# Kernel tuning notes

Hardware: AMD Instinct MI355X
Metric: run time of the kernel (lower is better)

## Reference

```python
import jax, jax.numpy as jnp
import numpy as np

N = 50000
E = 800000
NEG_SLOPE = 0.2


def gat_conv(x, W, att_src, att_dst, bias, src, dst, concat):
    """PyG GATConv (shared lin for src/dst, self-loops already included in src/dst).
    x: [N, Fin], W: [Fin, H*C], att_*: [H, C], bias: [H*C] if concat else [C].
    """
    H, C = att_src.shape
    h = (x @ W).reshape(N, H, C)                      # [N,H,C]
    a_src = jnp.sum(h * att_src[None], axis=-1)       # [N,H]
    a_dst = jnp.sum(h * att_dst[None], axis=-1)       # [N,H]
    alpha = a_src[src] + a_dst[dst]                   # [E,H]
    alpha = jax.nn.leaky_relu(alpha, NEG_SLOPE)
    # segment softmax over incoming edges of each destination node
    amax = jax.ops.segment_max(alpha, dst, num_segments=N)
    alpha = jnp.exp(alpha - amax[dst])
    denom = jax.ops.segment_sum(alpha, dst, num_segments=N)
    alpha = alpha / (denom[dst] + 1e-16)
    msg = h[src] * alpha[:, :, None]                  # [E,H,C]
    out = jax.ops.segment_sum(msg, dst, num_segments=N)  # [N,H,C]
    if concat:
        return out.reshape(N, H * C) + bias
    return out.mean(axis=1) + bias


def setup_inputs() -> dict:
    key = jax.random.key(0)
    ks = jax.random.split(key, 10)
    x = jax.random.normal(ks[0], (N, 64), dtype=jnp.float32)
    edge_index = jax.random.randint(ks[1], (2, E), 0, N, dtype=jnp.int32)
    s = 0.1
    # layer 1: in=64 -> heads=2, out=32, concat=True (width 64)
    W1 = jax.random.normal(ks[2], (64, 64), dtype=jnp.float32) * s
    att_src1 = jax.random.normal(ks[3], (2, 32), dtype=jnp.float32) * s
    att_dst1 = jax.random.normal(ks[4], (2, 32), dtype=jnp.float32) * s
    b1 = jnp.zeros((64,), dtype=jnp.float32)
    # recon: in=64 -> heads=2, out=64, concat=False
    W2 = jax.random.normal(ks[5], (64, 128), dtype=jnp.float32) * s
    att_src2 = jax.random.normal(ks[6], (2, 64), dtype=jnp.float32) * s
    att_dst2 = jax.random.normal(ks[7], (2, 64), dtype=jnp.float32) * s
    b2 = jnp.zeros((64,), dtype=jnp.float32)
    return {"x": x, "edge_index": edge_index,
            "W1": W1, "att_src1": att_src1, "att_dst1": att_dst1, "b1": b1,
            "W2": W2, "att_src2": att_src2, "att_dst2": att_dst2, "b2": b2}


def reference(x, edge_index, W1, att_src1, att_dst1, b1, W2, att_src2, att_dst2, b2):
    # add self loops (PyG GATConv default)
    loop = jnp.arange(N, dtype=edge_index.dtype)
    src = jnp.concatenate([edge_index[0], loop])
    dst = jnp.concatenate([edge_index[1], loop])
    h = gat_conv(x, W1, att_src1, att_dst1, b1, src, dst, concat=True)
    out = gat_conv(h, W2, att_src2, att_dst2, b2, src, dst, concat=False)
    return out
```

## Files before the change

### kernel.cpp

```cpp
#include <hip/hip_runtime.h>
#include <hip/hip_fp16.h>

#define NEG_SLOPE 0.2f
#define BCAP 6144

__device__ __forceinline__ float lrelu(float a) { return a > 0.f ? a : NEG_SLOPE * a; }

struct half4 { __half2 a, b; };
__device__ __forceinline__ half4 pack_half4(float4 v) {
    half4 r; r.a = __floats2half2_rn(v.x, v.y); r.b = __floats2half2_rn(v.z, v.w); return r;
}
__device__ __forceinline__ void unpack8(uint4 u, float* f) {
    const __half2* hp = (const __half2*)&u;
#pragma unroll
    for (int i = 0; i < 4; i++) {
        float2 t = __half22float2(hp[i]);
        f[2 * i] = t.x; f[2 * i + 1] = t.y;
    }
}
__device__ __forceinline__ void unpack4(uint2 u, float* f) {
    const __half2* hp = (const __half2*)&u;
#pragma unroll
    for (int i = 0; i < 2; i++) {
        float2 t = __half22float2(hp[i]);
        f[2 * i] = t.x; f[2 * i + 1] = t.y;
    }
}
__device__ __forceinline__ uint2 pack_half4f(const float* f) {
    uint2 u;
    __half2* hp = (__half2*)&u;
    hp[0] = __floats2half2_rn(f[0], f[1]);
    hp[1] = __floats2half2_rn(f[2], f[3]);
    return u;
}


__global__ __launch_bounds__(256) void init_va_kernel(int* __restrict__ bcur, int NBK,
                                                      const float* __restrict__ W2,
                                                      const float* __restrict__ att_s,
                                                      const float* __restrict__ att_d,
                                                      float* __restrict__ va_s,
                                                      float* __restrict__ va_d) {
    int t = threadIdx.x;
    if (t < NBK) bcur[t] = t * BCAP;
    int which = t >> 7;
    int h = (t >> 6) & 1, k = t & 63;
    const float* att = which ? att_d : att_s;
    float acc = 0.f;
    for (int c = 0; c < 64; c++)
        acc += W2[k * 128 + h * 64 + c] * att[h * 64 + c];
    (which ? va_d : va_s)[h * 64 + k] = acc;
}

__global__ __launch_bounds__(256) void bucketA_kernel(const int* __restrict__ ei, int E,
                                                      int Etot, int* __restrict__ bcur,
                                                      uint2* __restrict__ btmp) {
    __shared__ int lh[256];
    __shared__ int lbase[256];
    int t = threadIdx.x;
    int b0 = blockIdx.x * 4096;
    lh[t] = 0;
    __syncthreads();
    int s[16], d[16], bk[16];
#pragma unroll
    for (int i = 0; i < 16; i++) {
        int e = b0 + i * 256 + t;
        if (e < Etot) {
            int ss, dd;
            if (e < E) { ss = ei[e]; dd = ei[E + e]; }
            else       { ss = e - E; dd = ss; }
            s[i] = ss; d[i] = dd; bk[i] = dd >> 8;
            atomicAdd(&lh[bk[i]], 1);
        } else bk[i] = -1;
    }
    __syncthreads();
    if (lh[t] > 0) lbase[t] = atomicAdd(&bcur[t], lh[t]);
    __syncthreads();
    lh[t] = 0;
    __syncthreads();
#pragma unroll
    for (int i = 0; i < 16; i++) {
        if (bk[i] >= 0) {
            int pos = lbase[bk[i]] + atomicAdd(&lh[bk[i]], 1);
            btmp[pos] = make_uint2((unsigned)s[i], (unsigned)d[i]);
        }
    }
}

__global__ __launch_bounds__(256) void bucketB_kernel(const uint2* __restrict__ btmp,
                                                      const int* __restrict__ bcur,
                                                      int N, uint2* __restrict__ rowinfo,
                                                      int* __restrict__ csr) {
    __shared__ int lh[256];
    __shared__ int lbase[256];
    __shared__ int wsum[4];
    int bkt = blockIdx.x;
    int n0 = bkt << 8;
    int n1 = n0 + 256; if (n1 > N) n1 = N;
    int nn = n1 - n0;
    int t = threadIdx.x;
    lh[t] = 0;
    __syncthreads();
    int ebeg = bkt * BCAP;
    int eend = bcur[bkt];
    for (int e = ebeg + t; e < eend; e += 256)
        atomicAdd(&lh[(int)btmp[e].y - n0], 1);
    __syncthreads();
    int v = lh[t];
    int s = v;
    int lane = t & 63, w = t >> 6;
#pragma unroll
    for (int off = 1; off < 64; off <<= 1) {
        int x = __shfl_up(s, off, 64);
        if (lane >= off) s += x;
    }
    if (lane == 63) wsum[w] = s;
    __syncthreads();
    int woff = 0;
    if (w > 0) woff += wsum[0];
    if (w > 1) woff += wsum[1];
    if (w > 2) woff += wsum[2];
    int excl = woff + s - v;
    lbase[t] = ebeg + excl;
    if (t < nn) rowinfo[n0 + t] = make_uint2((unsigned)(ebeg + excl), (unsigned)v);
    lh[t] = 0;
    __syncthreads();
    for (int e = ebeg + t; e < eend; e += 256) {
        uint2 sd = btmp[e];
        int dl = (int)sd.y - n0;
        int slot = atomicAdd(&lh[dl], 1);
        csr[lbase[dl] + slot] = (int)sd.x;
    }
}


template <int M>
__global__ __launch_bounds__(256) void gemm64_kernel(const float* __restrict__ X,
                                                     const float* __restrict__ W,
                                                     __half* __restrict__ Yh,
                                                     const float* __restrict__ att_s,
                                                     const float* __restrict__ att_d,
                                                     float* __restrict__ a_src,
                                                     float* __restrict__ a_dst, int N) {
    constexpr int CG = M / 4;
    constexpr int RB = (256 / CG) * 2;
    constexpr int HL = CG / 2;
    __shared__ float4 ws[64 * CG];
    __shared__ float  xs[RB][68];
    int t = threadIdx.x;
    for (int i = t; i < 64 * CG; i += 256) ws[i] = ((const float4*)W)[i];
    int r0 = blockIdx.x * RB;
    for (int i = t; i < RB * 16; i += 256) {
        int r = i >> 4, k4 = i & 15;
        int row = r0 + r;
        float4 v = (row < N) ? ((const float4*)X)[(size_t)row * 16 + k4]
                             : make_float4(0.f, 0.f, 0.f, 0.f);
        ((float4*)&xs[r][0])[k4] = v;
    }
    __syncthreads();
    int c = t % CG;
    int rl = (t / CG) * 2;
    float4 a0 = make_float4(0.f, 0.f, 0.f, 0.f);
    float4 a1 = make_float4(0.f, 0.f, 0.f, 0.f);
#pragma unroll 8
    for (int k = 0; k < 64; k++) {
        float4 w = ws[k * CG + c];
        float x0 = xs[rl][k];
        float x1 = xs[rl + 1][k];
        a0.x = fmaf(x0, w.x, a0.x); a0.y = fmaf(x0, w.y, a0.y);
        a0.z = fmaf(x0, w.z, a0.z); a0.w = fmaf(x0, w.w, a0.w);
        a1.x = fmaf(x1, w.x, a1.x); a1.y = fmaf(x1, w.y, a1.y);
        a1.z = fmaf(x1, w.z, a1.z); a1.w = fmaf(x1, w.w, a1.w);
    }
    int row0 = r0 + rl;
    if (row0 < N)     ((half4*)Yh)[(size_t)row0 * CG + c] = pack_half4(a0);
    if (row0 + 1 < N) ((half4*)Yh)[(size_t)(row0 + 1) * CG + c] = pack_half4(a1);

    float4 s4 = ((const float4*)att_s)[c];
    float4 d4 = ((const float4*)att_d)[c];
    float vs0 = a0.x * s4.x + a0.y * s4.y + a0.z * s4.z + a0.w * s4.w;
    float vd0 = a0.x * d4.x + a0.y * d4.y + a0.z * d4.z + a0.w * d4.w;
    float vs1 = a1.x * s4.x + a1.y * s4.y + a1.z * s4.z + a1.w * s4.w;
    float vd1 = a1.x * d4.x + a1.y * d4.y + a1.z * d4.z + a1.w * d4.w;
#pragma unroll
    for (int off = 1; off < HL; off <<= 1) {
        vs0 += __shfl_xor(vs0, off, 64);
        vd0 += __shfl_xor(vd0, off, 64);
        vs1 += __shfl_xor(vs1, off, 64);
        vd1 += __shfl_xor(vd1, off, 64);
    }
    if ((c & (HL - 1)) == 0) {
        int hh = c / HL;
        if (row0 < N)     { a_src[row0 * 2 + hh] = vs0; a_dst[row0 * 2 + hh] = vd0; }
        if (row0 + 1 < N) { a_src[(row0 + 1) * 2 + hh] = vs1; a_dst[(row0 + 1) * 2 + hh] = vd1; }
    }
}


__device__ __forceinline__ void reg_softmax64(const float* __restrict__ asrc, float2 ad,
                                              const int* __restrict__ csr, int beg, int deg,
                                              int lane, int& sidx, float& w0n, float& w1n) {
    float a0 = -1e30f, a1 = -1e30f;
    sidx = 0;
    if (lane < deg) {
        sidx = csr[beg + lane];
        float2 as = ((const float2*)asrc)[sidx];
        a0 = lrelu(as.x + ad.x);
        a1 = lrelu(as.y + ad.y);
    }
    float m0 = a0, m1 = a1;
#pragma unroll
    for (int off = 32; off; off >>= 1) {
        m0 = fmaxf(m0, __shfl_xor(m0, off, 64));
        m1 = fmaxf(m1, __shfl_xor(m1, off, 64));
    }
    float w0 = (lane < deg) ? __expf(a0 - m0) : 0.f;
    float w1 = (lane < deg) ? __expf(a1 - m1) : 0.f;
    float d0 = w0, d1 = w1;
#pragma unroll
    for (int off = 32; off; off >>= 1) {
        d0 += __shfl_xor(d0, off, 64);
        d1 += __shfl_xor(d1, off, 64);
    }
    w0n = w0 / (d0 + 1e-16f);
    w1n = w1 / (d1 + 1e-16f);
}

__device__ __forceinline__ void reg_softmax32(const float* __restrict__ asrc, float2 ad,
                                              const int* __restrict__ csr, int beg, int deg,
                                              int hl, int& sidx, float& w0n, float& w1n) {
    float a0 = -1e30f, a1 = -1e30f;
    sidx = 0;
    if (hl < deg) {
        sidx = csr[beg + hl];
        float2 as = ((const float2*)asrc)[sidx];
        a0 = lrelu(as.x + ad.x);
        a1 = lrelu(as.y + ad.y);
    }
    float m0 = a0, m1 = a1;
#pragma unroll
    for (int off = 16; off; off >>= 1) {
        m0 = fmaxf(m0, __shfl_xor(m0, off, 64));
        m1 = fmaxf(m1, __shfl_xor(m1, off, 64));
    }
    float w0 = (hl < deg) ? __expf(a0 - m0) : 0.f;
    float w1 = (hl < deg) ? __expf(a1 - m1) : 0.f;
    float d0 = w0, d1 = w1;
#pragma unroll
    for (int off = 16; off; off >>= 1) {
        d0 += __shfl_xor(d0, off, 64);
        d1 += __shfl_xor(d1, off, 64);
    }
    w0n = w0 / (d0 + 1e-16f);
    w1n = w1 / (d1 + 1e-16f);
}


__device__ void concat_full64(const __half* __restrict__ hg, const float* __restrict__ asrc,
                              const float* __restrict__ adst, const uint2* __restrict__ rowinfo,
                              const int* __restrict__ csr, const float* __restrict__ bias,
                              __half* __restrict__ out1h, const float* __restrict__ vaS,
                              const float* __restrict__ vaD, float* __restrict__ asrc2,
                              float* __restrict__ adst2, int node, int lane) {
    uint2 ri = rowinfo[node];
    int beg = (int)ri.x, deg = (int)ri.y;
    int end = beg + deg;
    float2 ad = ((const float2*)adst)[node];
    int g = lane >> 4, q = lane & 15;
    float acc[4];
#pragma unroll
    for (int j = 0; j < 4; j++) acc[j] = 0.f;
    if (deg <= 64) {
        int sidx; float w0n, w1n;
        reg_softmax64(asrc, ad, csr, beg, deg, lane, sidx, w0n, w1n);
        for (int j0 = 0; j0 < deg; j0 += 4) {
            int j = j0 + g;
            int s = __shfl(sidx, j, 64);
            float wa = __shfl(w0n, j, 64);
            float wb = __shfl(w1n, j, 64);
            bool valid = j < deg;
            float w = valid ? ((q < 8) ? wa : wb) : 0.f;
            s = valid ? s : 0;
            uint2 u = ((const uint2*)(hg + (size_t)s * 64))[q];
            float f[4];
            unpack4(u, f);
#pragma unroll
            for (int k = 0; k < 4; k++) acc[k] = fmaf(f[k], w, acc[k]);
        }
    } else {
        float m0 = -1e30f, m1 = -1e30f;
        for (int i = lane; i < deg; i += 64) {
            int s = csr[beg + i];
            float2 as = ((const float2*)asrc)[s];
            m0 = fmaxf(m0, lrelu(as.x + ad.x));
            m1 = fmaxf(m1, lrelu(as.y + ad.y));
        }
#pragma unroll
        for (int off = 32; off; off >>= 1) {
            m0 = fmaxf(m0, __shfl_xor(m0, off, 64));
            m1 = fmaxf(m1, __shfl_xor(m1, off, 64));
        }
        float d0 = 0.f, d1 = 0.f;
        for (int i = lane; i < deg; i += 64) {
            int s = csr[beg + i];
            float2 as = ((const float2*)asrc)[s];
            d0 += __expf(lrelu(as.x + ad.x) - m0);
            d1 += __expf(lrelu(as.y + ad.y) - m1);
        }
#pragma unroll
        for (int off = 32; off; off >>= 1) {
            d0 += __shfl_xor(d0, off, 64);
            d1 += __shfl_xor(d1, off, 64);
        }
        float inv0 = 1.f / (d0 + 1e-16f), inv1 = 1.f / (d1 + 1e-16f);
        for (int e = beg + g; e < end; e += 4) {
            int s = csr[e];
            float2 as = ((const float2*)asrc)[s];
            float w = (q < 8) ? __expf(lrelu(as.x + ad.x) - m0) * inv0
                              : __expf(lrelu(as.y + ad.y) - m1) * inv1;
            uint2 u = ((const uint2*)(hg + (size_t)s * 64))[q];
            float f[4];
            unpack4(u, f);
#pragma unroll
            for (int k = 0; k < 4; k++) acc[k] = fmaf(f[k], w, acc[k]);
        }
    }
#pragma unroll
    for (int j = 0; j < 4; j++) {
        acc[j] += __shfl_xor(acc[j], 16, 64);
        acc[j] += __shfl_xor(acc[j], 32, 64);
    }
    float4 b = ((const float4*)bias)[q];
    acc[0] += b.x; acc[1] += b.y; acc[2] += b.z; acc[3] += b.w;
    if (lane < 16)
        ((uint2*)(out1h + (size_t)node * 64))[q] = pack_half4f(acc);
    float4 sA = ((const float4*)vaS)[q];
    float4 sB = ((const float4*)vaS)[16 + q];
    float4 dA = ((const float4*)vaD)[q];
    float4 dB = ((const float4*)vaD)[16 + q];
    float rs0 = acc[0] * sA.x + acc[1] * sA.y + acc[2] * sA.z + acc[3] * sA.w;
    float rs1 = acc[0] * sB.x + acc[1] * sB.y + acc[2] * sB.z + acc[3] * sB.w;
    float rd0 = acc[0] * dA.x + acc[1] * dA.y + acc[2] * dA.z + acc[3] * dA.w;
    float rd1 = acc[0] * dB.x + acc[1] * dB.y + acc[2] * dB.z + acc[3] * dB.w;
#pragma unroll
    for (int off = 1; off < 16; off <<= 1) {
        rs0 += __shfl_xor(rs0, off, 64);
        rs1 += __shfl_xor(rs1, off, 64);
        rd0 += __shfl_xor(rd0, off, 64);
        rd1 += __shfl_xor(rd1, off, 64);
    }
    if (lane == 0) {
        ((float2*)asrc2)[node] = make_float2(rs0, rs1);
        ((float2*)adst2)[node] = make_float2(rd0, rd1);
    }
}

__device__ void agg2_full64(const __half* __restrict__ xg, const float* __restrict__ asrc,
                            const float* __restrict__ adst, const uint2* __restrict__ rowinfo,
                            const int* __restrict__ csr, __half* __restrict__ aggcat,
                            int node, int lane) {
    uint2 ri = rowinfo[node];
    int beg = (int)ri.x, deg = (int)ri.y;
    int end = beg + deg;
    float2 ad = ((const float2*)adst)[node];
    int g = lane >> 4, q = lane & 15;
    float acc0[4], acc1[4];
#pragma unroll
    for (int j = 0; j < 4; j++) { acc0[j] = 0.f; acc1[j] = 0.f; }
    if (deg <= 64) {
        int sidx; float w0n, w1n;
        reg_softmax64(asrc, ad, csr, beg, deg, lane, sidx, w0n, w1n);
        for (int j0 = 0; j0 < deg; j0 += 4) {
            int j = j0 + g;
            int s = __shfl(sidx, j, 64);
            float wa = __shfl(w0n, j, 64);
            float wb = __shfl(w1n, j, 64);
            bool valid = j < deg;
            float w0 = valid ? wa : 0.f;
            float w1 = valid ? wb : 0.f;
            s = valid ? s : 0;
            uint2 u = ((const uint2*)(xg + (size_t)s * 64))[q];
            float f[4];
            unpack4(u, f);
#pragma unroll
            for (int k = 0; k < 4; k++) {
                acc0[k] = fmaf(f[k], w0, acc0[k]);
                acc1[k] = fmaf(f[k], w1, acc1[k]);
            }
        }
    } else {
        float m0 = -1e30f, m1 = -1e30f;
        for (int i = lane; i < deg; i += 64) {
            int s = csr[beg + i];
            float2 as = ((const float2*)asrc)[s];
            m0 = fmaxf(m0, lrelu(as.x + ad.x));
            m1 = fmaxf(m1, lrelu(as.y + ad.y));
        }
#pragma unroll
        for (int off = 32; off; off >>= 1) {
            m0 = fmaxf(m0, __shfl_xor(m0, off, 64));
            m1 = fmaxf(m1, __shfl_xor(m1, off, 64));
        }
        float d0 = 0.f, d1 = 0.f;
        for (int i = lane; i < deg; i += 64) {
            int s = csr[beg + i];
            float2 as = ((const float2*)asrc)[s];
            d0 += __expf(lrelu(as.x + ad.x) - m0);
            d1 += __expf(lrelu(as.y + ad.y) - m1);
        }
#pragma unroll
        for (int off = 32; off; off >>= 1) {
            d0 += __shfl_xor(d0, off, 64);
            d1 += __shfl_xor(d1, off, 64);
        }
        float inv0 = 1.f / (d0 + 1e-16f), inv1 = 1.f / (d1 + 1e-16f);
        for (int e = beg + g; e < end; e += 4) {
            int s = csr[e];
            float2 as = ((const float2*)asrc)[s];
            float w0 = __expf(lrelu(as.x + ad.x) - m0) * inv0;
            float w1 = __expf(lrelu(as.y + ad.y) - m1) * inv1;
            uint2 u = ((const uint2*)(xg + (size_t)s * 64))[q];
            float f[4];
            unpack4(u, f);
#pragma unroll
            for (int k = 0; k < 4; k++) {
                acc0[k] = fmaf(f[k], w0, acc0[k]);
                acc1[k] = fmaf(f[k], w1, acc1[k]);
            }
        }
    }
#pragma unroll
    for (int j = 0; j < 4; j++) {
        acc0[j] += __shfl_xor(acc0[j], 16, 64);
        acc0[j] += __shfl_xor(acc0[j], 32, 64);
        acc1[j] += __shfl_xor(acc1[j], 16, 64);
        acc1[j] += __shfl_xor(acc1[j], 32, 64);
    }
    if (lane < 16) {
        ((uint2*)(aggcat + (size_t)node * 128))[q] = pack_half4f(acc0);
        ((uint2*)(aggcat + (size_t)node * 128 + 64))[q] = pack_half4f(acc1);
    }
}


__global__ __launch_bounds__(256) void agg_sm_concat_kernel(const __half* __restrict__ hg,
                                                            const float* __restrict__ asrc,
                                                            const float* __restrict__ adst,
                                                            const uint2* __restrict__ rowinfo,
                                                            const int* __restrict__ csr,
                                                            const float* __restrict__ bias,
                                                            __half* __restrict__ out1h,
                                                            const float* __restrict__ vaS,
                                                            const float* __restrict__ vaD,
                                                            float* __restrict__ asrc2,
                                                            float* __restrict__ adst2, int N) {
    int nodeA = blockIdx.x * 8 + (threadIdx.x >> 6) * 2;
    if (nodeA >= N) return;
    int lane = threadIdx.x & 63;
    int half = lane >> 5, hl = lane & 31;
    int node = nodeA + half;
    bool nodeok = node < N;
    int nodec = nodeok ? node : nodeA;
    uint2 ri = rowinfo[nodec];
    int beg = (int)ri.x, deg = (int)ri.y;
    int degmax = max(deg, __shfl_xor(deg, 32, 64));

    if (degmax <= 32) {
        float2 ad = ((const float2*)adst)[nodec];
        int sidx; float w0n, w1n;
        reg_softmax32(asrc, ad, csr, beg, deg, hl, sidx, w0n, w1n);
        int g = hl >> 4, q = hl & 15;
        float acc[4];
#pragma unroll
        for (int j = 0; j < 4; j++) acc[j] = 0.f;
        for (int j0 = 0; j0 < degmax; j0 += 4) {
            int jA = j0 + g, jB = j0 + 2 + g;
            int slA = half * 32 + (jA < 31 ? jA : 31);
            int slB = half * 32 + (jB < 31 ? jB : 31);
            int sA = __shfl(sidx, slA, 64);
            float waA = __shfl(w0n, slA, 64);
            float wbA = __shfl(w1n, slA, 64);
            int sB = __shfl(sidx, slB, 64);
            float waB = __shfl(w0n, slB, 64);
            float wbB = __shfl(w1n, slB, 64);
            bool vA = jA < deg, vB = jB < deg;
            float wA = vA ? ((q < 8) ? waA : wbA) : 0.f;
            float wB = vB ? ((q < 8) ? waB : wbB) : 0.f;
            sA = vA ? sA : 0;
            sB = vB ? sB : 0;
            uint2 uA = ((const uint2*)(hg + (size_t)sA * 64))[q];
            uint2 uB = ((const uint2*)(hg + (size_t)sB * 64))[q];
            float fA[4], fB[4];
            unpack4(uA, fA);
            unpack4(uB, fB);
#pragma unroll
            for (int k = 0; k < 4; k++) acc[k] = fmaf(fA[k], wA, acc[k]);
#pragma unroll
            for (int k = 0; k < 4; k++) acc[k] = fmaf(fB[k], wB, acc[k]);
        }
#pragma unroll
        for (int j = 0; j < 4; j++) acc[j] += __shfl_xor(acc[j], 16, 64);
        float4 b = ((const float4*)bias)[q];
        acc[0] += b.x; acc[1] += b.y; acc[2] += b.z; acc[3] += b.w;
        if (nodeok && hl < 16)
            ((uint2*)(out1h + (size_t)node * 64))[q] = pack_half4f(acc);
        float4 sA4 = ((const float4*)vaS)[q];
        float4 sB4 = ((const float4*)vaS)[16 + q];
        float4 dA4 = ((const float4*)vaD)[q];
        float4 dB4 = ((const float4*)vaD)[16 + q];
        float rs0 = acc[0] * sA4.x + acc[1] * sA4.y + acc[2] * sA4.z + acc[3] * sA4.w;
        float rs1 = acc[0] * sB4.x + acc[1] * sB4.y + acc[2] * sB4.z + acc[3] * sB4.w;
        float rd0 = acc[0] * dA4.x + acc[1] * dA4.y + acc[2] * dA4.z + acc[3] * dA4.w;
        float rd1 = acc[0] * dB4.x + acc[1] * dB4.y + acc[2] * dB4.z + acc[3] * dB4.w;
#pragma unroll
        for (int off = 1; off < 16; off <<= 1) {
            rs0 += __shfl_xor(rs0, off, 64);
            rs1 += __shfl_xor(rs1, off, 64);
            rd0 += __shfl_xor(rd0, off, 64);
            rd1 += __shfl_xor(rd1, off, 64);
        }
        if (nodeok && hl == 0) {
            ((float2*)asrc2)[node] = make_float2(rs0, rs1);
            ((float2*)adst2)[node] = make_float2(rd0, rd1);
        }
    } else {
        concat_full64(hg, asrc, adst, rowinfo, csr, bias, out1h, vaS, vaD,
                      asrc2, adst2, nodeA, lane);
        if (nodeA + 1 < N)
            concat_full64(hg, asrc, adst, rowinfo, csr, bias, out1h, vaS, vaD,
                          asrc2, adst2, nodeA + 1, lane);
    }
}


__global__ __launch_bounds__(256) void agg_sm2_kernel(const __half* __restrict__ xg,
                                                      const float* __restrict__ asrc,
                                                      const float* __restrict__ adst,
                                                      const uint2* __restrict__ rowinfo,
                                                      const int* __restrict__ csr,
                                                      __half* __restrict__ aggcat, int N) {
    int nodeA = blockIdx.x * 8 + (threadIdx.x >> 6) * 2;
    if (nodeA >= N) return;
    int lane = threadIdx.x & 63;
    int half = lane >> 5, hl = lane & 31;
    int node = nodeA + half;
    bool nodeok = node < N;
    int nodec = nodeok ? node : nodeA;
    uint2 ri = rowinfo[nodec];
    int beg = (int)ri.x, deg = (int)ri.y;
    int degmax = max(deg, __shfl_xor(deg, 32, 64));

    if (degmax <= 32) {
        float2 ad = ((const float2*)adst)[nodec];
        int sidx; float w0n, w1n;
        reg_softmax32(asrc, ad, csr, beg, deg, hl, sidx, w0n, w1n);
        int g = hl >> 4, q = hl & 15;
        float acc0[4], acc1[4];
#pragma unroll
        for (int j = 0; j < 4; j++) { acc0[j] = 0.f; acc1[j] = 0.f; }
        for (int j0 = 0; j0 < degmax; j0 += 4) {
            int jA = j0 + g, jB = j0 + 2 + g;
            int slA = half * 32 + (jA < 31 ? jA : 31);
            int slB = half * 32 + (jB < 31 ? jB : 31);
            int sA = __shfl(sidx, slA, 64);
            float waA = __shfl(w0n, slA, 64);
            float wbA = __shfl(w1n, slA, 64);
            int sB = __shfl(sidx, slB, 64);
            float waB = __shfl(w0n, slB, 64);
            float wbB = __shfl(w1n, slB, 64);
            bool vA = jA < deg, vB = jB < deg;
            float w0A = vA ? waA : 0.f, w1A = vA ? wbA : 0.f;
            float w0B = vB ? waB : 0.f, w1B = vB ? wbB : 0.f;
            sA = vA ? sA : 0;
            sB = vB ? sB : 0;
            uint2 uA = ((const uint2*)(xg + (size_t)sA * 64))[q];
            uint2 uB = ((const uint2*)(xg + (size_t)sB * 64))[q];
            float fA[4], fB[4];
            unpack4(uA, fA);
            unpack4(uB, fB);
#pragma unroll
            for (int k = 0; k < 4; k++) {
                acc0[k] = fmaf(fA[k], w0A, acc0[k]);
                acc1[k] = fmaf(fA[k], w1A, acc1[k]);
            }
#pragma unroll
            for (int k = 0; k < 4; k++) {
                acc0[k] = fmaf(fB[k], w0B, acc0[k]);
                acc1[k] = fmaf(fB[k], w1B, acc1[k]);
            }
        }
#pragma unroll
        for (int j = 0; j < 4; j++) {
            acc0[j] += __shfl_xor(acc0[j], 16, 64);
            acc1[j] += __shfl_xor(acc1[j], 16, 64);
        }
        if (nodeok && hl < 16) {
            ((uint2*)(aggcat + (size_t)node * 128))[q] = pack_half4f(acc0);
            ((uint2*)(aggcat + (size_t)node * 128 + 64))[q] = pack_half4f(acc1);
        }
    } else {
        agg2_full64(xg, asrc, adst, rowinfo, csr, aggcat, nodeA, lane);
        if (nodeA + 1 < N)
            agg2_full64(xg, asrc, adst, rowinfo, csr, aggcat, nodeA + 1, lane);
    }
}


__global__ __launch_bounds__(256) void gemmK128_kernel(const __half* __restrict__ Xh,
                                                       const float* __restrict__ W2,
                                                       const float* __restrict__ bias,
                                                       float* __restrict__ Y, int N) {
    __shared__ float4 ws[128 * 16];
    __shared__ float  xs[32][132];
    int t = threadIdx.x;
    for (int i = t; i < 128 * 16; i += 256) {
        int k2 = i >> 4, c4 = i & 15;
        int k = k2 & 63, h = k2 >> 6;
        float4 w = ((const float4*)W2)[k * 32 + h * 16 + c4];
        w.x *= 0.5f; w.y *= 0.5f; w.z *= 0.5f; w.w *= 0.5f;
        ws[i] = w;
    }
    int r0 = blockIdx.x * 32;
    for (int i = t; i < 512; i += 256) {
        int r = i >> 4, j = i & 15;
        int row = r0 + r;
        uint4 u = make_uint4(0u, 0u, 0u, 0u);
        if (row < N) u = ((const uint4*)(Xh + (size_t)row * 128))[j];
        float f[8];
        unpack8(u, f);
#pragma unroll
        for (int jj = 0; jj < 8; jj++) xs[r][j * 8 + jj] = f[jj];
    }
    __syncthreads();
    int c = t & 15;
    int rl = (t >> 4) * 2;
    float4 a0 = make_float4(0.f, 0.f, 0.f, 0.f);
    float4 a1 = make_float4(0.f, 0.f, 0.f, 0.f);
#pragma unroll 8
    for (int k = 0; k < 128; k++) {
        float4 w = ws[k * 16 + c];
        float x0 = xs[rl][k];
        float x1 = xs[rl + 1][k];
        a0.x = fmaf(x0, w.x, a0.x); a0.y = fmaf(x0, w.y, a0.y);
        a0.z = fmaf(x0, w.z, a0.z); a0.w = fmaf(x0, w.w, a0.w);
        a1.x = fmaf(x1, w.x, a1.x); a1.y = fmaf(x1, w.y, a1.y);
        a1.z = fmaf(x1, w.z, a1.z); a1.w = fmaf(x1, w.w, a1.w);
    }
    float4 b = ((const float4*)bias)[c];
    a0.x += b.x; a0.y += b.y; a0.z += b.z; a0.w += b.w;
    a1.x += b.x; a1.y += b.y; a1.z += b.z; a1.w += b.w;
    int row0 = r0 + rl;
    if (row0 < N)     ((float4*)Y)[(size_t)row0 * 16 + c] = a0;
    if (row0 + 1 < N) ((float4*)Y)[(size_t)(row0 + 1) * 16 + c] = a1;
}


extern "C" void kernel_launch(void* const* d_in, const int* in_sizes, int n_in,
                              void* d_out, int out_size, void* d_ws, size_t ws_size,
                              hipStream_t stream) {
    const float* x        = (const float*)d_in[0];
    const int*   ei       = (const int*)d_in[1];
    const float* W1       = (const float*)d_in[2];
    const float* att_src1 = (const float*)d_in[3];
    const float* att_dst1 = (const float*)d_in[4];
    const float* b1       = (const float*)d_in[5];
    const float* W2       = (const float*)d_in[6];
    const float* att_src2 = (const float*)d_in[7];
    const float* att_dst2 = (const float*)d_in[8];
    const float* b2       = (const float*)d_in[9];
    float* out = (float*)d_out;

    const int N = in_sizes[0] / 64;
    const int E = in_sizes[1] / 2;
    const int Etot = E + N;
    const int NBK = (N + 255) >> 8;

    char* base = (char*)d_ws;
    size_t off = 0;
    auto alloc = [&](size_t bytes) -> char* {
        char* p = base + off;
        off = (off + bytes + 255) & ~(size_t)255;
        return p;
    };
    int*    bcur    = (int*)alloc((size_t)NBK * 4);
    uint2*  rowinfo = (uint2*)alloc((size_t)N * 8);
    int*    csr     = (int*)alloc((size_t)NBK * BCAP * 4);
    uint2*  btmp    = (uint2*)alloc((size_t)NBK * BCAP * 8);
    __half* h1g     = (__half*)alloc((size_t)N * 64 * 2);
    float*  asrc1   = (float*)alloc((size_t)N * 2 * 4);
    float*  adst1   = (float*)alloc((size_t)N * 2 * 4);
    __half* out1h   = (__half*)alloc((size_t)N * 64 * 2);
    __half* aggcat  = (__half*)alloc((size_t)N * 128 * 2);
    float*  asrc2   = (float*)alloc((size_t)N * 2 * 4);
    float*  adst2   = (float*)alloc((size_t)N * 2 * 4);
    float*  vaS     = (float*)alloc(128 * 4);
    float*  vaD     = (float*)alloc(128 * 4);
    (void)ws_size; (void)n_in; (void)out_size;

    const int nba = (Etot + 4095) / 4096;
    const int nb8 = (N + 7) / 8;

    init_va_kernel<<<1, 256, 0, stream>>>(bcur, NBK, W2, att_src2, att_dst2, vaS, vaD);
    bucketA_kernel<<<nba, 256, 0, stream>>>(ei, E, Etot, bcur, btmp);
    bucketB_kernel<<<NBK, 256, 0, stream>>>(btmp, bcur, N, rowinfo, csr);

    gemm64_kernel<64><<<(N + 31) / 32, 256, 0, stream>>>(x, W1, h1g, att_src1, att_dst1,
                                                         asrc1, adst1, N);
    agg_sm_concat_kernel<<<nb8, 256, 0, stream>>>(h1g, asrc1, adst1, rowinfo, csr, b1,
                                                  out1h, vaS, vaD, asrc2, adst2, N);

    agg_sm2_kernel<<<nb8, 256, 0, stream>>>(out1h, asrc2, adst2, rowinfo, csr, aggcat, N);
    gemmK128_kernel<<<(N + 31) / 32, 256, 0, stream>>>(aggcat, W2, b2, out, N);
}
```

Measured before the change: 117.8 us.

## Pack bucket edges into 32 bits, half-pack softmax weights, widen gather unroll

Bucketed edges are stored as one 32-bit word (16-bit source plus 8-bit local destination) instead of a uint2, halving the temp traffic in the CSR build. Softmax weights for both heads are packed into one fp16 pair so one shuffle replaces two. The aggregation loops now issue four neighbour row gathers per iteration instead of two, to raise memory-level parallelism. This assumes node indices fit in 16 bits and lowers weight precision to fp16.

Measured after the change: 117.5 us. About the same (-0.3%).

```diff
diff --git a/kernel.cpp b/kernel.cpp
--- a/kernel.cpp
+++ b/kernel.cpp
@@ -32,6 +32,13 @@
     hp[0] = __floats2half2_rn(f[0], f[1]);
     hp[1] = __floats2half2_rn(f[2], f[3]);
     return u;
+}
+__device__ __forceinline__ unsigned pack_w2(float w0, float w1) {
+    __half2 h = __floats2half2_rn(w0, w1);
+    return *(unsigned*)&h;
+}
+__device__ __forceinline__ float2 unpack_w2(unsigned u) {
+    return __half22float2(*(__half2*)&u);
 }
 
 
@@ -54,14 +61,14 @@
 
 __global__ __launch_bounds__(256) void bucketA_kernel(const int* __restrict__ ei, int E,
                                                       int Etot, int* __restrict__ bcur,
-                                                      uint2* __restrict__ btmp) {
+                                                      unsigned* __restrict__ btmp) {
     __shared__ int lh[256];
     __shared__ int lbase[256];
     int t = threadIdx.x;
     int b0 = blockIdx.x * 4096;
     lh[t] = 0;
     __syncthreads();
-    int s[16], d[16], bk[16];
+    int s[16], dl[16], bk[16];
 #pragma unroll
     for (int i = 0; i < 16; i++) {
         int e = b0 + i * 256 + t;
@@ -69,7 +76,7 @@
             int ss, dd;
             if (e < E) { ss = ei[e]; dd = ei[E + e]; }
             else       { ss = e - E; dd = ss; }
-            s[i] = ss; d[i] = dd; bk[i] = dd >> 8;
+            s[i] = ss; dl[i] = dd & 255; bk[i] = dd >> 8;
             atomicAdd(&lh[bk[i]], 1);
         } else bk[i] = -1;
     }
@@ -82,12 +89,12 @@
     for (int i = 0; i < 16; i++) {
         if (bk[i] >= 0) {
             int pos = lbase[bk[i]] + atomicAdd(&lh[bk[i]], 1);
-            btmp[pos] = make_uint2((unsigned)s[i], (unsigned)d[i]);
-        }
-    }
-}
-
-__global__ __launch_bounds__(256) void bucketB_kernel(const uint2* __restrict__ btmp,
+            btmp[pos] = (unsigned)s[i] | ((unsigned)dl[i] << 16);
+        }
+    }
+}
+
+__global__ __launch_bounds__(256) void bucketB_kernel(const unsigned* __restrict__ btmp,
                                                       const int* __restrict__ bcur,
                                                       int N, uint2* __restrict__ rowinfo,
                                                       int* __restrict__ csr) {
@@ -104,7 +111,7 @@
     int ebeg = bkt * BCAP;
     int eend = bcur[bkt];
     for (int e = ebeg + t; e < eend; e += 256)
-        atomicAdd(&lh[(int)btmp[e].y - n0], 1);
+        atomicAdd(&lh[(btmp[e] >> 16) & 255], 1);
     __syncthreads();
     int v = lh[t];
     int s = v;
@@ -126,10 +133,10 @@
     lh[t] = 0;
     __syncthreads();
     for (int e = ebeg + t; e < eend; e += 256) {
-        uint2 sd = btmp[e];
-        int dl = (int)sd.y - n0;
+        unsigned u = btmp[e];
+        int dl = (u >> 16) & 255;
         int slot = atomicAdd(&lh[dl], 1);
-        csr[lbase[dl] + slot] = (int)sd.x;
+        csr[lbase[dl] + slot] = (int)(u & 0xFFFFu);
     }
 }
 
@@ -226,9 +233,9 @@
     w1n = w1 / (d1 + 1e-16f);
 }
 
-__device__ __forceinline__ void reg_softmax32(const float* __restrict__ asrc, float2 ad,
-                                              const int* __restrict__ csr, int beg, int deg,
-                                              int hl, int& sidx, float& w0n, float& w1n) {
+__device__ __forceinline__ void reg_softmax32p(const float* __restrict__ asrc, float2 ad,
+                                               const int* __restrict__ csr, int beg, int deg,
+                                               int hl, int& sidx, unsigned& pw) {
     float a0 = -1e30f, a1 = -1e30f;
     sidx = 0;
     if (hl < deg) {
@@ -251,8 +258,7 @@
         d0 += __shfl_xor(d0, off, 64);
         d1 += __shfl_xor(d1, off, 64);
     }
-    w0n = w0 / (d0 + 1e-16f);
-    w1n = w1 / (d1 + 1e-16f);
+    pw = pack_w2(w0 / (d0 + 1e-16f), w1 / (d1 + 1e-16f));
 }
 
 
@@ -467,36 +473,40 @@
 
     if (degmax <= 32) {
         float2 ad = ((const float2*)adst)[nodec];
-        int sidx; float w0n, w1n;
-        reg_softmax32(asrc, ad, csr, beg, deg, hl, sidx, w0n, w1n);
+        int sidx; unsigned pw;
+        reg_softmax32p(asrc, ad, csr, beg, deg, hl, sidx, pw);
         int g = hl >> 4, q = hl & 15;
         float acc[4];
 #pragma unroll
         for (int j = 0; j < 4; j++) acc[j] = 0.f;
-        for (int j0 = 0; j0 < degmax; j0 += 4) {
-            int jA = j0 + g, jB = j0 + 2 + g;
-            int slA = half * 32 + (jA < 31 ? jA : 31);
-            int slB = half * 32 + (jB < 31 ? jB : 31);
-            int sA = __shfl(sidx, slA, 64);
-            float waA = __shfl(w0n, slA, 64);
-            float wbA = __shfl(w1n, slA, 64);
-            int sB = __shfl(sidx, slB, 64);
-            float waB = __shfl(w0n, slB, 64);
-            float wbB = __shfl(w1n, slB, 64);
-            bool vA = jA < deg, vB = jB < deg;
-            float wA = vA ? ((q < 8) ? waA : wbA) : 0.f;
-            float wB = vB ? ((q < 8) ? waB : wbB) : 0.f;
-            sA = vA ? sA : 0;
-            sB = vB ? sB : 0;
-            uint2 uA = ((const uint2*)(hg + (size_t)sA * 64))[q];
-            uint2 uB = ((const uint2*)(hg + (size_t)sB * 64))[q];
-            float fA[4], fB[4];
-            unpack4(uA, fA);
-            unpack4(uB, fB);
-#pragma unroll
-            for (int k = 0; k < 4; k++) acc[k] = fmaf(fA[k], wA, acc[k]);
-#pragma unroll
-            for (int k = 0; k < 4; k++) acc[k] = fmaf(fB[k], wB, acc[k]);
+        for (int j0 = 0; j0 < degmax; j0 += 8) {
+            int jj[4], ss[4];
+            unsigned pp[4];
+#pragma unroll
+            for (int p = 0; p < 4; p++) {
+                int j = j0 + 2 * p + g;
+                jj[p] = j;
+                int sl = half * 32 + (j < 31 ? j : 31);
+                ss[p] = __shfl(sidx, sl, 64);
+                pp[p] = __shfl((int)pw, sl, 64);
+            }
+            uint2 uu[4];
+            float ww[4];
+#pragma unroll
+            for (int p = 0; p < 4; p++) {
+                bool valid = jj[p] < deg;
+                float2 wv = unpack_w2(pp[p]);
+                ww[p] = valid ? ((q < 8) ? wv.x : wv.y) : 0.f;
+                int s = valid ? ss[p] : 0;
+                uu[p] = ((const uint2*)(hg + (size_t)s * 64))[q];
+            }
+#pragma unroll
+            for (int p = 0; p < 4; p++) {
+                float f[4];
+                unpack4(uu[p], f);
+#pragma unroll
+                for (int k = 0; k < 4; k++) acc[k] = fmaf(f[k], ww[p], acc[k]);
+            }
         }
 #pragma unroll
         for (int j = 0; j < 4; j++) acc[j] += __shfl_xor(acc[j], 16, 64);
@@ -552,41 +562,43 @@
 
     if (degmax <= 32) {
         float2 ad = ((const float2*)adst)[nodec];
-        int sidx; float w0n, w1n;
-        reg_softmax32(asrc, ad, csr, beg, deg, hl, sidx, w0n, w1n);
+        int sidx; unsigned pw;
+        reg_softmax32p(asrc, ad, csr, beg, deg, hl, sidx, pw);
         int g = hl >> 4, q = hl & 15;
         float acc0[4], acc1[4];
 #pragma unroll
         for (int j = 0; j < 4; j++) { acc0[j] = 0.f; acc1[j] = 0.f; }
-        for (int j0 = 0; j0 < degmax; j0 += 4) {
-            int jA = j0 + g, jB = j0 + 2 + g;
-            int slA = half * 32 + (jA < 31 ? jA : 31);
-            int slB = half * 32 + (jB < 31 ? jB : 31);
-            int sA = __shfl(sidx, slA, 64);
-            float waA = __shfl(w0n, slA, 64);
-            float wbA = __shfl(w1n, slA, 64);
-            int sB = __shfl(sidx, slB, 64);
-            float waB = __shfl(w0n, slB, 64);
-            float wbB = __shfl(w1n, slB, 64);
-            bool vA = jA < deg, vB = jB < deg;
-            float w0A = vA ? waA : 0.f, w1A = vA ? wbA : 0.f;
-            float w0B = vB ? waB : 0.f, w1B = vB ? wbB : 0.f;
-            sA = vA ? sA : 0;
-            sB = vB ? sB : 0;
-            uint2 uA = ((const uint2*)(xg + (size_t)sA * 64))[q];
-            uint2 uB = ((const uint2*)(xg + (size_t)sB * 64))[q];
-            float fA[4], fB[4];
-            unpack4(uA, fA);
-            unpack4(uB, fB);
-#pragma unroll
-            for (int k = 0; k < 4; k++) {
-                acc0[k] = fmaf(fA[k], w0A, acc0[k]);
-                acc1[k] = fmaf(fA[k], w1A, acc1[k]);
+        for (int j0 = 0; j0 < degmax; j0 += 8) {
+            int jj[4], ss[4];
+            unsigned pp[4];
+#pragma unroll
+            for (int p = 0; p < 4; p++) {
+                int j = j0 + 2 * p + g;
+                jj[p] = j;
+                int sl = half * 32 + (j < 31 ? j : 31);
+                ss[p] = __shfl(sidx, sl, 64);
+                pp[p] = __shfl((int)pw, sl, 64);
             }
-#pragma unroll
-            for (int k = 0; k < 4; k++) {
-                acc0[k] = fmaf(fB[k], w0B, acc0[k]);
-                acc1[k] = fmaf(fB[k], w1B, acc1[k]);
+            uint2 uu[4];
+            float w0a[4], w1a[4];
+#pragma unroll
+            for (int p = 0; p < 4; p++) {
+                bool valid = jj[p] < deg;
+                float2 wv = unpack_w2(pp[p]);
+                w0a[p] = valid ? wv.x : 0.f;
+                w1a[p] = valid ? wv.y : 0.f;
+                int s = valid ? ss[p] : 0;
+                uu[p] = ((const uint2*)(xg + (size_t)s * 64))[q];
+            }
+#pragma unroll
+            for (int p = 0; p < 4; p++) {
+                float f[4];
+                unpack4(uu[p], f);
+#pragma unroll
+                for (int k = 0; k < 4; k++) {
+                    acc0[k] = fmaf(f[k], w0a[p], acc0[k]);
+                    acc1[k] = fmaf(f[k], w1a[p], acc1[k]);
+                }
             }
         }
 #pragma unroll
@@ -682,19 +694,19 @@
         off = (off + bytes + 255) & ~(size_t)255;
         return p;
     };
-    int*    bcur    = (int*)alloc((size_t)NBK * 4);
-    uint2*  rowinfo = (uint2*)alloc((size_t)N * 8);
-    int*    csr     = (int*)alloc((size_t)NBK * BCAP * 4);
-    uint2*  btmp    = (uint2*)alloc((size_t)NBK * BCAP * 8);
-    __half* h1g     = (__half*)alloc((size_t)N * 64 * 2);
-    float*  asrc1   = (float*)alloc((size_t)N * 2 * 4);
-    float*  adst1   = (float*)alloc((size_t)N * 2 * 4);
-    __half* out1h   = (__half*)alloc((size_t)N * 64 * 2);
-    __half* aggcat  = (__half*)alloc((size_t)N * 128 * 2);
-    float*  asrc2   = (float*)alloc((size_t)N * 2 * 4);
-    float*  adst2   = (float*)alloc((size_t)N * 2 * 4);
-    float*  vaS     = (float*)alloc(128 * 4);
-    float*  vaD     = (float*)alloc(128 * 4);
+    int*      bcur    = (int*)alloc((size_t)NBK * 4);
+    uint2*    rowinfo = (uint2*)alloc((size_t)N * 8);
+    int*      csr     = (int*)alloc((size_t)NBK * BCAP * 4);
+    unsigned* btmp    = (unsigned*)alloc((size_t)NBK * BCAP * 4);
+    __half*   h1g     = (__half*)alloc((size_t)N * 64 * 2);
+    float*    asrc1   = (float*)alloc((size_t)N * 2 * 4);
+    float*    adst1   = (float*)alloc((size_t)N * 2 * 4);
+    __half*   out1h   = (__half*)alloc((size_t)N * 64 * 2);
+    __half*   aggcat  = (__half*)alloc((size_t)N * 128 * 2);
+    float*    asrc2   = (float*)alloc((size_t)N * 2 * 4);
+    float*    adst2   = (float*)alloc((size_t)N * 2 * 4);
+    float*    vaS     = (float*)alloc(128 * 4);
+    float*    vaD     = (float*)alloc(128 * 4);
     (void)ws_size; (void)n_in; (void)out_size;
 
     const int nba = (Etot + 4095) / 4096;
```
